# Optimization experiments

Hardware: AMD Instinct MI355X
Metric: run time of the kernel (lower is better)

## Reference

```python
import jax, jax.numpy as jnp
import numpy as np

B, L, D = 2, 512, 1024
INNER = 32
PAIR = 128


def setup_inputs() -> dict:
    key = jax.random.key(0)
    ks = jax.random.split(key, 6)
    scale = lambda fan_in: 1.0 / np.sqrt(fan_in)
    return {
        "sequence_state": jax.random.normal(ks[0], (B, L, D), dtype=jnp.float32),
        "ln_gamma": jnp.ones((D,), dtype=jnp.float32),
        "ln_beta": jnp.zeros((D,), dtype=jnp.float32),
        "W_proj": jax.random.normal(ks[1], (2 * INNER, D), dtype=jnp.float32) * scale(D),
        "b_proj": jnp.zeros((2 * INNER,), dtype=jnp.float32),
        "W_o": jax.random.normal(ks[2], (PAIR, 2 * INNER), dtype=jnp.float32) * scale(2 * INNER),
        "b_o": jnp.zeros((PAIR,), dtype=jnp.float32),
    }


def reference(sequence_state, ln_gamma, ln_beta, W_proj, b_proj, W_o, b_o):
    eps = 1e-5
    # LayerNorm over last dim
    mu = jnp.mean(sequence_state, axis=-1, keepdims=True)
    var = jnp.mean(jnp.square(sequence_state - mu), axis=-1, keepdims=True)
    s = (sequence_state - mu) * jax.lax.rsqrt(var + eps) * ln_gamma + ln_beta
    # proj: B x L x 2*inner
    s = jnp.einsum("bld,ed->ble", s, W_proj) + b_proj
    q, k = jnp.split(s, 2, axis=-1)  # each B x L x inner
    # broadcast outer product / difference: B x L x L x inner
    prod = q[:, None, :, :] * k[:, :, None, :]
    diff = q[:, None, :, :] - k[:, :, None, :]
    x = jnp.concatenate([prod, diff], axis=-1)  # B x L x L x 2*inner
    # o_proj: B x L x L x pairwise
    x = jnp.einsum("bije,pe->bijp", x, W_o) + b_o
    return x
```

## Files before the change

kernel.cpp:

```cpp
#include <hip/hip_runtime.h>
#include <hip/hip_bf16.h>
#include <stdint.h>


typedef __attribute__((ext_vector_type(8))) short short8;
typedef __attribute__((ext_vector_type(4))) float floatx4;

__device__ __forceinline__ unsigned short f2bf(float f) {
    union { float f; unsigned int u; } v; v.f = f;
    return (unsigned short)((v.u + 0x7FFFu + ((v.u >> 16) & 1u)) >> 16);
}

__device__ __forceinline__ floatx4 fmadd4(float s, floatx4 w, floatx4 a) {
    a.x += s * w.x; a.y += s * w.y; a.z += s * w.z; a.w += s * w.w; return a;
}

__global__ __launch_bounds__(256) void k0_transpose(
    const float* __restrict__ Wproj, const float* __restrict__ Wo,
    float* __restrict__ Wt, float* __restrict__ Wdt)
{
    int g = blockIdx.x * 256 + threadIdx.x;
    if (g < 65536) {
        int o = g >> 10, d = g & 1023;
        Wt[d * 64 + o] = Wproj[g];
    } else {
        int h = g - 65536;
        int e = h >> 7, p = h & 127;
        Wdt[h] = Wo[p * 64 + 32 + e];
    }
}

__global__ __launch_bounds__(256) void k1_ln_proj(
    const float* __restrict__ x, const float* __restrict__ gamma, const float* __restrict__ beta,
    const float* __restrict__ Wt, const float* __restrict__ b_proj,
    const float* __restrict__ Wdt, const float* __restrict__ b_o,
    unsigned short* __restrict__ Qbf, float* __restrict__ Kf, float* __restrict__ C0)
{
    __shared__ __attribute__((aligned(16))) float s_sh[4][1024];
    __shared__ __attribute__((aligned(16))) float part[4][16][68];
    __shared__ float k_sh[4][32];

    const int t = threadIdx.x;
    const int w = t >> 6;
    const int lane = t & 63;
    const int row = blockIdx.x * 4 + w;

    const float* xr = x + (size_t)row * 1024;
    floatx4 xv[4];
    float sum = 0.f, sq = 0.f;
#pragma unroll
    for (int c = 0; c < 4; ++c) {
        xv[c] = *(const floatx4*)(xr + (c * 64 + lane) * 4);
        sum += xv[c].x + xv[c].y + xv[c].z + xv[c].w;
        sq  += xv[c].x * xv[c].x + xv[c].y * xv[c].y + xv[c].z * xv[c].z + xv[c].w * xv[c].w;
    }
#pragma unroll
    for (int m = 1; m < 64; m <<= 1) {
        sum += __shfl_xor(sum, m, 64);
        sq  += __shfl_xor(sq,  m, 64);
    }
    const float mu   = sum * (1.f / 1024.f);
    const float var  = sq * (1.f / 1024.f) - mu * mu;
    const float rsig = rsqrtf(var + 1e-5f);
#pragma unroll
    for (int c = 0; c < 4; ++c) {
        int d = (c * 64 + lane) * 4;
        floatx4 g4 = *(const floatx4*)(gamma + d);
        floatx4 b4 = *(const floatx4*)(beta + d);
        floatx4 s4;
        s4.x = (xv[c].x - mu) * rsig * g4.x + b4.x;
        s4.y = (xv[c].y - mu) * rsig * g4.y + b4.y;
        s4.z = (xv[c].z - mu) * rsig * g4.z + b4.z;
        s4.w = (xv[c].w - mu) * rsig * g4.w + b4.w;
        *(floatx4*)(&s_sh[w][d]) = s4;
    }
    __syncthreads();

    {
        const int o4 = t & 15;
        const int ch = t >> 4;
        const floatx4* Wt4 = (const floatx4*)Wt;
        floatx4 a0 = {0.f, 0.f, 0.f, 0.f}, a1 = a0, a2 = a0, a3 = a0;
        const int dbase = ch * 64;
#pragma unroll 8
        for (int dd = 0; dd < 64; ++dd) {
            const int d = dbase + dd;
            floatx4 w4 = Wt4[d * 16 + o4];
            a0 = fmadd4(s_sh[0][d], w4, a0);
            a1 = fmadd4(s_sh[1][d], w4, a1);
            a2 = fmadd4(s_sh[2][d], w4, a2);
            a3 = fmadd4(s_sh[3][d], w4, a3);
        }
        *(floatx4*)&part[0][ch][o4 * 4] = a0;
        *(floatx4*)&part[1][ch][o4 * 4] = a1;
        *(floatx4*)&part[2][ch][o4 * 4] = a2;
        *(floatx4*)&part[3][ch][o4 * 4] = a3;
    }
    __syncthreads();

    {
        const int r = t >> 6, oo = t & 63;
        float v = b_proj[oo];
#pragma unroll
        for (int c = 0; c < 16; ++c) v += part[r][c][oo];
        const int rowr = blockIdx.x * 4 + r;
        if (oo < 32) {
            Qbf[rowr * 32 + oo] = f2bf(v);
        } else {
            Kf[rowr * 32 + (oo - 32)] = v;
            k_sh[r][oo - 32] = v;
        }
    }
    __syncthreads();

    {
        const int p = t & 127;
        const int r0 = t >> 7;
#pragma unroll
        for (int rr = 0; rr < 2; ++rr) {
            const int r = r0 * 2 + rr;
            float a = 0.f;
#pragma unroll 8
            for (int e = 0; e < 32; ++e) a += k_sh[r][e] * Wdt[e * 128 + p];
            C0[(size_t)(blockIdx.x * 4 + r) * 128 + p] = b_o[p] - a;
        }
    }
}

__global__ __launch_bounds__(256, 4) void k2_pair(
    const unsigned short* __restrict__ Qbf, const float* __restrict__ Kf,
    const float* __restrict__ C0, const float* __restrict__ Wo,
    float* __restrict__ out)
{
    __shared__ __attribute__((aligned(16))) unsigned short G2[128 * 40];

    const int t  = threadIdx.x;
    const int bi = blockIdx.x;
    const int b  = bi >> 9;

    {
        const int p  = t >> 1;
        const int eh = (t & 1) * 16;
        const float* kp = Kf + (size_t)bi * 32 + eh;
        const float* wp = Wo + p * 64 + eh;
        unsigned short g[16];
#pragma unroll
        for (int c = 0; c < 4; ++c) {
            floatx4 kc  = *(const floatx4*)(kp + c * 4);
            floatx4 wpc = *(const floatx4*)(wp + c * 4);
            floatx4 wdc = *(const floatx4*)(wp + 32 + c * 4);
            g[c * 4 + 0] = f2bf(kc.x * wpc.x + wdc.x);
            g[c * 4 + 1] = f2bf(kc.y * wpc.y + wdc.y);
            g[c * 4 + 2] = f2bf(kc.z * wpc.z + wdc.z);
            g[c * 4 + 3] = f2bf(kc.w * wpc.w + wdc.w);
        }
        short8 lo, hi;
#pragma unroll
        for (int u = 0; u < 8; ++u) { lo[u] = (short)g[u]; hi[u] = (short)g[8 + u]; }
        *(short8*)(&G2[p * 40 + eh])     = lo;
        *(short8*)(&G2[p * 40 + eh + 8]) = hi;
    }
    __syncthreads();

    const int wave = t >> 6, lane = t & 63;
    const int col = lane & 15, quad = lane >> 4;

    short8 gfrag[8];
#pragma unroll
    for (int pt = 0; pt < 8; ++pt)
        gfrag[pt] = *(const short8*)(&G2[(pt * 16 + col) * 40 + quad * 8]);

    floatx4 cv[8];
#pragma unroll
    for (int pt = 0; pt < 8; ++pt)
        cv[pt] = *(const floatx4*)(C0 + (size_t)bi * 128 + pt * 16 + quad * 4);

    float* outb = out + (size_t)bi * (512 * 128) + (size_t)col * 128 + quad * 4;
    const unsigned short* qb = Qbf + ((size_t)b * 512 + col) * 32 + quad * 8;

    for (int l = 0; l < 8; ++l) {
        const int j0 = (wave * 8 + l) * 16;
        const short8 afrag = *(const short8*)(qb + (size_t)j0 * 32);
        float* orow = outb + (size_t)j0 * 128;
#pragma unroll
        for (int pt = 0; pt < 8; ++pt) {
            floatx4 acc = __builtin_amdgcn_mfma_f32_16x16x32_bf16(gfrag[pt], afrag, cv[pt], 0, 0, 0);
            __builtin_nontemporal_store(acc, (floatx4*)(orow + pt * 16));
        }
    }
}

extern "C" void kernel_launch(void* const* d_in, const int* in_sizes, int n_in,
                              void* d_out, int out_size, void* d_ws, size_t ws_size,
                              hipStream_t stream) {
    const float* x     = (const float*)d_in[0];
    const float* gamma = (const float*)d_in[1];
    const float* beta  = (const float*)d_in[2];
    const float* Wproj = (const float*)d_in[3];
    const float* bproj = (const float*)d_in[4];
    const float* Wo    = (const float*)d_in[5];
    const float* bo    = (const float*)d_in[6];
    float* out = (float*)d_out;

    float* ws = (float*)d_ws;
    float* Wt  = ws;
    float* Wdt = ws + 65536;
    float* Kf  = ws + 69632;
    float* C0  = ws + 102400;
    unsigned short* Qbf = (unsigned short*)(ws + 233472);

    hipLaunchKernelGGL(k0_transpose, dim3(272), dim3(256), 0, stream,
                       Wproj, Wo, Wt, Wdt);
    hipLaunchKernelGGL(k1_ln_proj, dim3(256), dim3(256), 0, stream,
                       x, gamma, beta, Wt, bproj, Wdt, bo, Qbf, Kf, C0);
    hipLaunchKernelGGL(k2_pair, dim3(1024), dim3(256), 0, stream,
                       Qbf, Kf, C0, Wo, out);
}
```

Before: 326.5 us.

## Precompute per-row bf16 G matrices in LN kernel and prefetch Q fragments in pair kernel

The per-row bf16 G matrix (k*Wo_prod + Wo_diff) is now built in the LayerNorm/projection kernel and written to a global workspace buffer. The pair kernel no longer does this work itself, along with its shared-memory staging and __syncthreads. The pair kernel now loads G fragments straight from global memory and software-prefetches the next Q fragment in its loop. The cost is an extra 8 MB of G written and read back through memory. The main kernel is dominated by its 268 MB output store, so the expected change is small.

```diff
diff --git a/kernel.cpp b/kernel.cpp
--- a/kernel.cpp
+++ b/kernel.cpp
@@ -34,7 +34,9 @@
     const float* __restrict__ x, const float* __restrict__ gamma, const float* __restrict__ beta,
     const float* __restrict__ Wt, const float* __restrict__ b_proj,
     const float* __restrict__ Wdt, const float* __restrict__ b_o,
-    unsigned short* __restrict__ Qbf, float* __restrict__ Kf, float* __restrict__ C0)
+    const float* __restrict__ Wo,
+    unsigned short* __restrict__ Qbf, float* __restrict__ C0,
+    unsigned short* __restrict__ Gall)
 {
     __shared__ __attribute__((aligned(16))) float s_sh[4][1024];
     __shared__ __attribute__((aligned(16))) float part[4][16][68];
@@ -107,7 +109,6 @@
         if (oo < 32) {
             Qbf[rowr * 32 + oo] = f2bf(v);
         } else {
-            Kf[rowr * 32 + (oo - 32)] = v;
             k_sh[r][oo - 32] = v;
         }
     }
@@ -125,68 +126,74 @@
             C0[(size_t)(blockIdx.x * 4 + r) * 128 + p] = b_o[p] - a;
         }
     }
+
+    {
+        const int p  = t >> 1;
+        const int eh = (t & 1) * 16;
+        const float* wp = Wo + p * 64 + eh;
+        floatx4 wpc[4], wdc[4];
+#pragma unroll
+        for (int c = 0; c < 4; ++c) {
+            wpc[c] = *(const floatx4*)(wp + c * 4);
+            wdc[c] = *(const floatx4*)(wp + 32 + c * 4);
+        }
+#pragma unroll
+        for (int r = 0; r < 4; ++r) {
+            unsigned short g[16];
+#pragma unroll
+            for (int c = 0; c < 4; ++c) {
+#pragma unroll
+                for (int u = 0; u < 4; ++u) {
+                    float kv = k_sh[r][eh + c * 4 + u];
+                    g[c * 4 + u] = f2bf(kv * wpc[c][u] + wdc[c][u]);
+                }
+            }
+            short8 lo, hi;
+#pragma unroll
+            for (int u = 0; u < 8; ++u) { lo[u] = (short)g[u]; hi[u] = (short)g[8 + u]; }
+            unsigned short* gr = Gall + (size_t)(blockIdx.x * 4 + r) * 4096 + p * 32 + eh;
+            *(short8*)(gr)     = lo;
+            *(short8*)(gr + 8) = hi;
+        }
+    }
 }
 
 __global__ __launch_bounds__(256, 4) void k2_pair(
-    const unsigned short* __restrict__ Qbf, const float* __restrict__ Kf,
-    const float* __restrict__ C0, const float* __restrict__ Wo,
-    float* __restrict__ out)
+    const unsigned short* __restrict__ Qbf, const unsigned short* __restrict__ Gall,
+    const float* __restrict__ C0, float* __restrict__ out)
 {
-    __shared__ __attribute__((aligned(16))) unsigned short G2[128 * 40];
-
     const int t  = threadIdx.x;
     const int bi = blockIdx.x;
     const int b  = bi >> 9;
-
-    {
-        const int p  = t >> 1;
-        const int eh = (t & 1) * 16;
-        const float* kp = Kf + (size_t)bi * 32 + eh;
-        const float* wp = Wo + p * 64 + eh;
-        unsigned short g[16];
-#pragma unroll
-        for (int c = 0; c < 4; ++c) {
-            floatx4 kc  = *(const floatx4*)(kp + c * 4);
-            floatx4 wpc = *(const floatx4*)(wp + c * 4);
-            floatx4 wdc = *(const floatx4*)(wp + 32 + c * 4);
-            g[c * 4 + 0] = f2bf(kc.x * wpc.x + wdc.x);
-            g[c * 4 + 1] = f2bf(kc.y * wpc.y + wdc.y);
-            g[c * 4 + 2] = f2bf(kc.z * wpc.z + wdc.z);
-            g[c * 4 + 3] = f2bf(kc.w * wpc.w + wdc.w);
-        }
-        short8 lo, hi;
-#pragma unroll
-        for (int u = 0; u < 8; ++u) { lo[u] = (short)g[u]; hi[u] = (short)g[8 + u]; }
-        *(short8*)(&G2[p * 40 + eh])     = lo;
-        *(short8*)(&G2[p * 40 + eh + 8]) = hi;
-    }
-    __syncthreads();
-
     const int wave = t >> 6, lane = t & 63;
     const int col = lane & 15, quad = lane >> 4;
 
+    const unsigned short* gb = Gall + (size_t)bi * 4096 + (size_t)col * 32 + quad * 8;
     short8 gfrag[8];
 #pragma unroll
     for (int pt = 0; pt < 8; ++pt)
-        gfrag[pt] = *(const short8*)(&G2[(pt * 16 + col) * 40 + quad * 8]);
+        gfrag[pt] = *(const short8*)(gb + pt * 512);
 
     floatx4 cv[8];
 #pragma unroll
     for (int pt = 0; pt < 8; ++pt)
         cv[pt] = *(const floatx4*)(C0 + (size_t)bi * 128 + pt * 16 + quad * 4);
 
-    float* outb = out + (size_t)bi * (512 * 128) + (size_t)col * 128 + quad * 4;
-    const unsigned short* qb = Qbf + ((size_t)b * 512 + col) * 32 + quad * 8;
-
+    const unsigned short* qp = Qbf + ((size_t)b * 512 + wave * 128 + col) * 32 + quad * 8;
+    float* orow = out + (size_t)bi * (512 * 128) + (size_t)(wave * 128 + col) * 128 + quad * 4;
+
+    short8 a_cur = *(const short8*)qp;
+#pragma unroll 1
     for (int l = 0; l < 8; ++l) {
-        const int j0 = (wave * 8 + l) * 16;
-        const short8 afrag = *(const short8*)(qb + (size_t)j0 * 32);
-        float* orow = outb + (size_t)j0 * 128;
+        short8 a_nxt = a_cur;
+        if (l < 7) a_nxt = *(const short8*)(qp + (size_t)(l + 1) * 512);
 #pragma unroll
         for (int pt = 0; pt < 8; ++pt) {
-            floatx4 acc = __builtin_amdgcn_mfma_f32_16x16x32_bf16(gfrag[pt], afrag, cv[pt], 0, 0, 0);
+            floatx4 acc = __builtin_amdgcn_mfma_f32_16x16x32_bf16(gfrag[pt], a_cur, cv[pt], 0, 0, 0);
             __builtin_nontemporal_store(acc, (floatx4*)(orow + pt * 16));
         }
+        orow += 16 * 128;
+        a_cur = a_nxt;
     }
 }
 
@@ -205,14 +212,14 @@
     float* ws = (float*)d_ws;
     float* Wt  = ws;
     float* Wdt = ws + 65536;
-    float* Kf  = ws + 69632;
-    float* C0  = ws + 102400;
-    unsigned short* Qbf = (unsigned short*)(ws + 233472);
+    float* C0  = ws + 69632;
+    unsigned short* Qbf  = (unsigned short*)(ws + 200704);
+    unsigned short* Gall = (unsigned short*)(ws + 217088);
 
     hipLaunchKernelGGL(k0_transpose, dim3(272), dim3(256), 0, stream,
                        Wproj, Wo, Wt, Wdt);
     hipLaunchKernelGGL(k1_ln_proj, dim3(256), dim3(256), 0, stream,
-                       x, gamma, beta, Wt, bproj, Wdt, bo, Qbf, Kf, C0);
+                       x, gamma, beta, Wt, bproj, Wdt, bo, Wo, Qbf, C0, Gall);
     hipLaunchKernelGGL(k2_pair, dim3(1024), dim3(256), 0, stream,
-                       Qbf, Kf, C0, Wo, out);
-}
+                       Qbf, Gall, C0, out);
+}
```

After: 325.3 us. About the same (-0.4%).
